# Optimization experiments

Measured on AMD Instinct MI355X. Metric: run time of the kernel, lower is better.

The kernel has to match this reference:

```python
import jax, jax.numpy as jnp
import numpy as np

EPS_LOG = 1e-08   # module eps (added inside log)
EPS_PD = 1e-06    # torch.nn.PairwiseDistance default eps (added to the difference)


def setup_inputs() -> dict:
    key = jax.random.key(0)
    x = jax.random.normal(key, (8192, 512), dtype=jnp.float32)
    return {"x": x}


def reference(x) -> jnp.ndarray:
    n = x.shape[0]
    # Cosine/dot similarity matrix [n, n]; mask the diagonal with -1 so a
    # point cannot be its own nearest neighbor.
    dots = x @ x.T
    idx = jnp.arange(n)
    dots = dots.at[idx, idx].set(-1.0)
    # Nearest neighbor (by dot product) per row; indices — no gradient path.
    I = jnp.argmax(dots, axis=1)
    # PairwiseDistance(p=2): ||x - x[I] + eps||_2 per row.
    diff = x - x[I] + EPS_PD
    rho = jnp.sqrt(jnp.sum(diff * diff, axis=1))
    loss = -jnp.mean(jnp.log(rho + EPS_LOG))
    return loss
```

## Files before the change

kernel.cpp:

```cpp
#include <hip/hip_runtime.h>


#define NPTS 8192
#define DIM  512
#define BM   128
#define BN   128
#define NTIL 64
#define NBLK (NTIL * (NTIL + 1) / 2)
#define KT_N 8

typedef float f32x16 __attribute__((ext_vector_type(16)));
typedef int   i32x4  __attribute__((ext_vector_type(4)));
typedef int   i32x8  __attribute__((ext_vector_type(8)));

__device__ __forceinline__ unsigned char f32_to_e4m3(float f) {
  unsigned u = __builtin_bit_cast(unsigned, f);
  unsigned s = (u >> 24) & 0x80u;
  unsigned a = u & 0x7FFFFFFFu;
  float af = __builtin_bit_cast(float, a);
  if (af < 0.015625f) {
    int m = (int)rintf(af * 512.0f);
    return (unsigned char)(s | (unsigned)m);
  }
  unsigned u2 = a + 0x0007FFFFu + ((a >> 20) & 1u);
  int e = (int)(u2 >> 23) - 127 + 7;
  unsigned m = (u2 >> 20) & 7u;
  if (e > 15) return (unsigned char)(s | 0x7Eu);
  return (unsigned char)(s | ((unsigned)e << 3) | m);
}

__device__ __forceinline__ unsigned int mono_f32(float f) {
  unsigned u = __builtin_bit_cast(unsigned, f);
  return u ^ (0x80000000u | (unsigned)((int)u >> 31));
}

__global__ void cvt_fp8_kernel(const float* __restrict__ x,
                               unsigned char* __restrict__ xq,
                               unsigned* __restrict__ nn32) {
  int i = blockIdx.x * blockDim.x + threadIdx.x;
  const float4* xp = reinterpret_cast<const float4*>(x) + 2 * (size_t)i;
  float4 v0 = xp[0], v1 = xp[1];
  unsigned long long w =
      (unsigned long long)f32_to_e4m3(v0.x) |
      ((unsigned long long)f32_to_e4m3(v0.y) << 8) |
      ((unsigned long long)f32_to_e4m3(v0.z) << 16) |
      ((unsigned long long)f32_to_e4m3(v0.w) << 24) |
      ((unsigned long long)f32_to_e4m3(v1.x) << 32) |
      ((unsigned long long)f32_to_e4m3(v1.y) << 40) |
      ((unsigned long long)f32_to_e4m3(v1.z) << 48) |
      ((unsigned long long)f32_to_e4m3(v1.w) << 56);
  reinterpret_cast<unsigned long long*>(xq)[i] = w;
  if (i < NPTS) nn32[i] = 0u;
}

__device__ __forceinline__ void gload_lds16(const unsigned char* g,
                                            unsigned char* l) {
  __builtin_amdgcn_global_load_lds(
      (__attribute__((address_space(1))) const void*)g,
      (__attribute__((address_space(3))) void*)l, 16, 0, 0);
}

__device__ __forceinline__ unsigned umax(unsigned a, unsigned b) {
  return a > b ? a : b;
}

__global__ __launch_bounds__(256, 3) void tri_gemm_kernel(
    const unsigned char* __restrict__ xq,
    unsigned* __restrict__ nn32) {
  __shared__ unsigned char lds[3][16384];

  const int orig = (int)blockIdx.x;
  int b = (orig & 7) * (NBLK >> 3) + (orig >> 3);
  int ti = (int)((sqrtf(8.0f * (float)b + 1.0f) - 1.0f) * 0.5f);
  while ((ti + 1) * (ti + 2) / 2 <= b) ++ti;
  while (ti * (ti + 1) / 2 > b) --ti;
  const int tj = b - ti * (ti + 1) / 2;

  const int tid  = (int)threadIdx.x;
  const int wid  = tid >> 6;
  const int lane = tid & 63;
  const int wr   = wid >> 1;
  const int wc   = wid & 1;
  const int l31  = lane & 31;
  const int h    = lane >> 5;
  const int arow0 = ti * BM;
  const int bcol0 = tj * BN;

#define STAGE(bufi, kt) do {                                                 \
    _Pragma("unroll")                                                        \
    for (int i_ = 0; i_ < 2; ++i_) {                                         \
      const int chunk_ = (i_ << 8) + tid;                        \
      const int row_   = chunk_ >> 2;                            \
      const int f_     = ((row_ >> 1) + (row_ >> 3)) & 3;                    \
      const int c_     = ((chunk_ & 3) - f_) & 3;                            \
      gload_lds16(xq + (size_t)(arow0 + row_) * DIM + (kt) * 64 + (c_ << 4), \
                  &lds[bufi][chunk_ << 4]);                                   \
      gload_lds16(xq + (size_t)(bcol0 + row_) * DIM + (kt) * 64 + (c_ << 4), \
                  &lds[bufi][8192 + (chunk_ << 4)]);                          \
    }                                                                        \
  } while (0)

  const int fr  = ((l31 >> 1) + (l31 >> 3)) & 3;
  const int s0  = (2 * h + fr) & 3;
  const int s1  = (2 * h + 1 + fr) & 3;
  const int abase = (wr * 64 + l31) * 64;
  const int bbase = 8192 + (wc * 64 + l31) * 64;
  const int aoff0 = abase + (s0 << 4), aoff1 = abase + (s1 << 4);
  const int boff0 = bbase + (s0 << 4), boff1 = bbase + (s1 << 4);

  f32x16 acc[2][2];
#pragma unroll
  for (int mi = 0; mi < 2; ++mi)
#pragma unroll
    for (int ni = 0; ni < 2; ++ni)
#pragma unroll
      for (int r = 0; r < 16; ++r) acc[mi][ni][r] = 0.f;

  STAGE(0, 0);
  STAGE(1, 1);

  for (int u = 0; u < KT_N; ++u) {
    const int cur = u - (u / 3) * 3;
    if (u == KT_N - 1) {
      asm volatile("s_waitcnt vmcnt(0)" ::: "memory");
    } else {
      asm volatile("s_waitcnt vmcnt(4)" ::: "memory");
    }
    asm volatile("s_barrier" ::: "memory");
    if (u + 2 < KT_N) {
      const int nb = (u + 2) - ((u + 2) / 3) * 3;
      STAGE(nb, u + 2);
    }

    i32x8 a8[2], b8[2];
#pragma unroll
    for (int mi = 0; mi < 2; ++mi) {
      i32x4 lo = *reinterpret_cast<const i32x4*>(&lds[cur][aoff0 + mi * 2048]);
      i32x4 hi = *reinterpret_cast<const i32x4*>(&lds[cur][aoff1 + mi * 2048]);
      a8[mi] = (i32x8){lo[0], lo[1], lo[2], lo[3], hi[0], hi[1], hi[2], hi[3]};
    }
#pragma unroll
    for (int ni = 0; ni < 2; ++ni) {
      i32x4 lo = *reinterpret_cast<const i32x4*>(&lds[cur][boff0 + ni * 2048]);
      i32x4 hi = *reinterpret_cast<const i32x4*>(&lds[cur][boff1 + ni * 2048]);
      b8[ni] = (i32x8){lo[0], lo[1], lo[2], lo[3], hi[0], hi[1], hi[2], hi[3]};
    }
    __builtin_amdgcn_s_setprio(1);
#pragma unroll
    for (int mi = 0; mi < 2; ++mi)
#pragma unroll
      for (int ni = 0; ni < 2; ++ni)
        acc[mi][ni] = __builtin_amdgcn_mfma_scale_f32_32x32x64_f8f6f4(
            a8[mi], b8[ni], acc[mi][ni], 0, 0,
            0, 0x7F7F7F7F, 0, 0x7F7F7F7F);
    __builtin_amdgcn_s_setprio(0);
  }
#undef STAGE

  const bool diagw = (ti == tj) && (wr == wc);

  unsigned M[2][2][16];
#pragma unroll
  for (int mi = 0; mi < 2; ++mi)
#pragma unroll
    for (int ni = 0; ni < 2; ++ni)
#pragma unroll
      for (int r = 0; r < 16; ++r)
        M[mi][ni][r] = mono_f32(acc[mi][ni][r]) & 0xFFFFE000u;

  unsigned K[32];
  const unsigned jb = 8191u - (unsigned)(bcol0 + wc * 64 + l31);
#pragma unroll
  for (int mi = 0; mi < 2; ++mi)
#pragma unroll
    for (int r = 0; r < 16; ++r) {
      const int rl = (r & 3) + 8 * (r >> 2) + 4 * h;
      unsigned best = 0u;
#pragma unroll
      for (int ni = 0; ni < 2; ++ni) {
        unsigned kk = M[mi][ni][r] | (jb - (unsigned)(ni * 32));
        if (diagw && mi == ni && rl == l31) kk = 0u;
        best = umax(best, kk);
      }
      K[mi * 16 + r] = best;
    }
#pragma unroll
  for (int k = 0; k < 5; ++k) {
    const int m = 1 << k;
    const unsigned kb = (unsigned)(lane >> k) & 1u;
#pragma unroll
    for (int i = 0; i < (16 >> k); ++i) {
      unsigned lo = K[2 * i], hi = K[2 * i + 1];
      unsigned keep = kb ? hi : lo;
      unsigned send = kb ? lo : hi;
      unsigned recv = (unsigned)__shfl_xor((int)send, m);
      K[i] = umax(keep, recv);
    }
  }
  {
    const int s = l31;
    const int gi = arow0 + wr * 64 + (s >> 4) * 32 +
                   ((s & 3) + 8 * ((s & 15) >> 2) + 4 * h);
    atomicMax(&nn32[gi], K[0]);
  }

  {
    unsigned C0 = 0u, C1 = 0u;
    const unsigned ib = 8191u - (unsigned)(arow0 + wr * 64);
#pragma unroll
    for (int mi = 0; mi < 2; ++mi)
#pragma unroll
      for (int r = 0; r < 16; ++r) {
        const int rl = (r & 3) + 8 * (r >> 2) + 4 * h;
        const unsigned idxk = ib - (unsigned)(mi * 32 + rl);
        unsigned k0 = M[mi][0][r] | idxk;
        if (diagw && mi == 0 && rl == l31) k0 = 0u;
        C0 = umax(C0, k0);
        unsigned k1 = M[mi][1][r] | idxk;
        if (diagw && mi == 1 && rl == l31) k1 = 0u;
        C1 = umax(C1, k1);
      }
    unsigned keep = h ? C1 : C0;
    unsigned send = h ? C0 : C1;
    unsigned recv = (unsigned)__shfl_xor((int)send, 32);
    unsigned R = umax(keep, recv);
    const int gj = bcol0 + wc * 64 + h * 32 + l31;
    atomicMax(&nn32[gj], R);
  }
}

__global__ void dist_log_kernel(const float* __restrict__ x,
                                const unsigned* __restrict__ nn32,
                                float* __restrict__ logs) {
  const int row  = blockIdx.x * 4 + ((int)threadIdx.x >> 6);
  const int lane = (int)threadIdx.x & 63;
  const int nn   = 8191 - (int)(nn32[row] & 8191u);
  const float4* xr = reinterpret_cast<const float4*>(x + (size_t)row * DIM);
  const float4* xn = reinterpret_cast<const float4*>(x + (size_t)nn  * DIM);
  float s = 0.f;
#pragma unroll
  for (int i = 0; i < 2; ++i) {
    float4 a = xr[lane + i * 64];
    float4 b = xn[lane + i * 64];
    float d0 = a.x - b.x + 1e-6f;
    float d1 = a.y - b.y + 1e-6f;
    float d2 = a.z - b.z + 1e-6f;
    float d3 = a.w - b.w + 1e-6f;
    s += d0 * d0 + d1 * d1 + d2 * d2 + d3 * d3;
  }
#pragma unroll
  for (int m = 32; m >= 1; m >>= 1) s += __shfl_xor(s, m);
  if (lane == 0) logs[row] = logf(sqrtf(s) + 1e-8f);
}

__global__ void final_reduce_kernel(const float* __restrict__ logs,
                                    float* __restrict__ out) {
  __shared__ float sm[1024];
  const int t = (int)threadIdx.x;
  float s = 0.f;
#pragma unroll
  for (int i = 0; i < 8; ++i) s += logs[t * 8 + i];
  sm[t] = s;
  __syncthreads();
  for (int k = 512; k > 0; k >>= 1) {
    if (t < k) sm[t] += sm[t + k];
    __syncthreads();
  }
  if (t == 0) out[0] = -(sm[0] / (float)NPTS);
}

extern "C" void kernel_launch(void* const* d_in, const int* in_sizes, int n_in,
                              void* d_out, int out_size, void* d_ws, size_t ws_size,
                              hipStream_t stream) {
  const float* x = (const float*)d_in[0];
  float* out = (float*)d_out;
  char* ws = (char*)d_ws;

  unsigned char* xq   = (unsigned char*)(ws);
  unsigned*      nn32 = (unsigned*)(ws + 4194304);
  float*         logs = (float*)(ws + 4227072);

  cvt_fp8_kernel<<<(NPTS * DIM / 8) / 256, 256, 0, stream>>>(x, xq, nn32);

  tri_gemm_kernel<<<NBLK, 256, 0, stream>>>(xq, nn32);

  dist_log_kernel<<<NPTS / 4, 256, 0, stream>>>(x, nn32, logs);

  final_reduce_kernel<<<1, 1024, 0, stream>>>(logs, out);
}
```

Before: 45.83 us.

## Switch K-loop to double-buffered 128-wide stages with fewer barriers

Replaces the triple-buffered 64-wide K pipeline (8 iterations, prefetch distance 2) with a double-buffered pipeline whose stages cover 128 bytes of K (4 iterations, prefetch distance 1). The goal is to halve the number of barriers and waitcnt points per tile and issue larger load batches. In exchange each iteration waits with vmcnt(0), so less load latency overlaps with compute, and LDS grows from 48KB to 64KB, which may cut occupancy below the three blocks per CU the launch bounds request.

```diff
diff --git a/kernel.cpp b/kernel.cpp
--- a/kernel.cpp
+++ b/kernel.cpp
@@ -7,7 +7,7 @@
 #define BN   128
 #define NTIL 64
 #define NBLK (NTIL * (NTIL + 1) / 2)
-#define KT_N 8
+#define MT_N 4
 
 typedef float f32x16 __attribute__((ext_vector_type(16)));
 typedef int   i32x4  __attribute__((ext_vector_type(4)));
@@ -67,7 +67,7 @@
 __global__ __launch_bounds__(256, 3) void tri_gemm_kernel(
     const unsigned char* __restrict__ xq,
     unsigned* __restrict__ nn32) {
-  __shared__ unsigned char lds[3][16384];
+  __shared__ unsigned char lds[2][32768];
 
   const int orig = (int)blockIdx.x;
   int b = (orig & 7) * (NBLK >> 3) + (orig >> 3);
@@ -86,17 +86,21 @@
   const int arow0 = ti * BM;
   const int bcol0 = tj * BN;
 
-#define STAGE(bufi, kt) do {                                                 \
+#define STAGE2(bufi, mt) do {                                                \
     _Pragma("unroll")                                                        \
-    for (int i_ = 0; i_ < 2; ++i_) {                                         \
-      const int chunk_ = (i_ << 8) + tid;                        \
-      const int row_   = chunk_ >> 2;                            \
-      const int f_     = ((row_ >> 1) + (row_ >> 3)) & 3;                    \
-      const int c_     = ((chunk_ & 3) - f_) & 3;                            \
-      gload_lds16(xq + (size_t)(arow0 + row_) * DIM + (kt) * 64 + (c_ << 4), \
-                  &lds[bufi][chunk_ << 4]);                                   \
-      gload_lds16(xq + (size_t)(bcol0 + row_) * DIM + (kt) * 64 + (c_ << 4), \
-                  &lds[bufi][8192 + (chunk_ << 4)]);                          \
+    for (int q_ = 0; q_ < 2; ++q_) {                                         \
+      _Pragma("unroll")                                                      \
+      for (int i_ = 0; i_ < 2; ++i_) {                                       \
+        const int chunk_ = (i_ << 8) + tid;                      \
+        const int row_   = chunk_ >> 2;                          \
+        const int f_     = ((row_ >> 1) + (row_ >> 3)) & 3;                  \
+        const int c_     = ((chunk_ & 3) - f_) & 3;                          \
+        const size_t go_ = (size_t)(mt) * 128 + q_ * 64 + (c_ << 4);         \
+        gload_lds16(xq + (size_t)(arow0 + row_) * DIM + go_,                 \
+                    &lds[bufi][q_ * 16384 + (chunk_ << 4)]);                  \
+        gload_lds16(xq + (size_t)(bcol0 + row_) * DIM + go_,                 \
+                    &lds[bufi][q_ * 16384 + 8192 + (chunk_ << 4)]);           \
+      }                                                                      \
     }                                                                        \
   } while (0)
 
@@ -116,46 +120,48 @@
 #pragma unroll
       for (int r = 0; r < 16; ++r) acc[mi][ni][r] = 0.f;
 
-  STAGE(0, 0);
-  STAGE(1, 1);
-
-  for (int u = 0; u < KT_N; ++u) {
-    const int cur = u - (u / 3) * 3;
-    if (u == KT_N - 1) {
-      asm volatile("s_waitcnt vmcnt(0)" ::: "memory");
-    } else {
-      asm volatile("s_waitcnt vmcnt(4)" ::: "memory");
+  STAGE2(0, 0);
+
+  for (int u = 0; u < MT_N; ++u) {
+    const int cur = u & 1;
+    asm volatile("s_waitcnt vmcnt(0)" ::: "memory");
+    asm volatile("s_barrier" ::: "memory");
+    if (u + 1 < MT_N) STAGE2(cur ^ 1, u + 1);
+
+#pragma unroll
+    for (int q = 0; q < 2; ++q) {
+      const int qb = q * 16384;
+      i32x8 a8[2], b8[2];
+#pragma unroll
+      for (int mi = 0; mi < 2; ++mi) {
+        i32x4 lo = *reinterpret_cast<const i32x4*>(
+            &lds[cur][qb + aoff0 + mi * 2048]);
+        i32x4 hi = *reinterpret_cast<const i32x4*>(
+            &lds[cur][qb + aoff1 + mi * 2048]);
+        a8[mi] = (i32x8){lo[0], lo[1], lo[2], lo[3],
+                         hi[0], hi[1], hi[2], hi[3]};
+      }
+#pragma unroll
+      for (int ni = 0; ni < 2; ++ni) {
+        i32x4 lo = *reinterpret_cast<const i32x4*>(
+            &lds[cur][qb + boff0 + ni * 2048]);
+        i32x4 hi = *reinterpret_cast<const i32x4*>(
+            &lds[cur][qb + boff1 + ni * 2048]);
+        b8[ni] = (i32x8){lo[0], lo[1], lo[2], lo[3],
+                         hi[0], hi[1], hi[2], hi[3]};
+      }
+      __builtin_amdgcn_s_setprio(1);
+#pragma unroll
+      for (int mi = 0; mi < 2; ++mi)
+#pragma unroll
+        for (int ni = 0; ni < 2; ++ni)
+          acc[mi][ni] = __builtin_amdgcn_mfma_scale_f32_32x32x64_f8f6f4(
+              a8[mi], b8[ni], acc[mi][ni], 0, 0,
+              0, 0x7F7F7F7F, 0, 0x7F7F7F7F);
+      __builtin_amdgcn_s_setprio(0);
     }
-    asm volatile("s_barrier" ::: "memory");
-    if (u + 2 < KT_N) {
-      const int nb = (u + 2) - ((u + 2) / 3) * 3;
-      STAGE(nb, u + 2);
-    }
-
-    i32x8 a8[2], b8[2];
-#pragma unroll
-    for (int mi = 0; mi < 2; ++mi) {
-      i32x4 lo = *reinterpret_cast<const i32x4*>(&lds[cur][aoff0 + mi * 2048]);
-      i32x4 hi = *reinterpret_cast<const i32x4*>(&lds[cur][aoff1 + mi * 2048]);
-      a8[mi] = (i32x8){lo[0], lo[1], lo[2], lo[3], hi[0], hi[1], hi[2], hi[3]};
-    }
-#pragma unroll
-    for (int ni = 0; ni < 2; ++ni) {
-      i32x4 lo = *reinterpret_cast<const i32x4*>(&lds[cur][boff0 + ni * 2048]);
-      i32x4 hi = *reinterpret_cast<const i32x4*>(&lds[cur][boff1 + ni * 2048]);
-      b8[ni] = (i32x8){lo[0], lo[1], lo[2], lo[3], hi[0], hi[1], hi[2], hi[3]};
-    }
-    __builtin_amdgcn_s_setprio(1);
-#pragma unroll
-    for (int mi = 0; mi < 2; ++mi)
-#pragma unroll
-      for (int ni = 0; ni < 2; ++ni)
-        acc[mi][ni] = __builtin_amdgcn_mfma_scale_f32_32x32x64_f8f6f4(
-            a8[mi], b8[ni], acc[mi][ni], 0, 0,
-            0, 0x7F7F7F7F, 0, 0x7F7F7F7F);
-    __builtin_amdgcn_s_setprio(0);
-  }
-#undef STAGE
+  }
+#undef STAGE2
 
   const bool diagw = (ti == tj) && (wr == wc);
 
```

Measured after the change: 50.33 us. +9.8%, slower.

## Switch triangular GEMM to single-wave 64x64 tiles with barrier-free double buffering

Applied to the files above, without the earlier changes.

Changes the triangular fp8 GEMM from 128x128 tiles run by four waves to 64x64 tiles run by one 64-lane wave, with a two-stage LDS buffer and no block barrier. Precomputed load pointers replace the per-stage address math, and the prefetch into the current buffer is issued after its LDS reads complete. The aim is to remove barrier sync and triangle-edge waste and to raise block count and occupancy. The cost is less operand reuse per block, so global and L2 traffic roughly doubles, and there are more atomicMax calls.

```diff
diff --git a/kernel.cpp b/kernel.cpp
--- a/kernel.cpp
+++ b/kernel.cpp
@@ -3,9 +3,8 @@
 
 #define NPTS 8192
 #define DIM  512
-#define BM   128
-#define BN   128
-#define NTIL 64
+#define BT   64
+#define NTIL 128
 #define NBLK (NTIL * (NTIL + 1) / 2)
 #define KT_N 8
 
@@ -64,10 +63,10 @@
   return a > b ? a : b;
 }
 
-__global__ __launch_bounds__(256, 3) void tri_gemm_kernel(
+__global__ __launch_bounds__(64, 3) void tri_gemm_kernel(
     const unsigned char* __restrict__ xq,
     unsigned* __restrict__ nn32) {
-  __shared__ unsigned char lds[3][16384];
+  __shared__ unsigned char lds[2][8192];
 
   const int orig = (int)blockIdx.x;
   int b = (orig & 7) * (NBLK >> 3) + (orig >> 3);
@@ -76,37 +75,39 @@
   while (ti * (ti + 1) / 2 > b) --ti;
   const int tj = b - ti * (ti + 1) / 2;
 
-  const int tid  = (int)threadIdx.x;
-  const int wid  = tid >> 6;
-  const int lane = tid & 63;
-  const int wr   = wid >> 1;
-  const int wc   = wid & 1;
+  const int lane = (int)threadIdx.x;
   const int l31  = lane & 31;
   const int h    = lane >> 5;
-  const int arow0 = ti * BM;
-  const int bcol0 = tj * BN;
+  const int arow0 = ti * BT;
+  const int bcol0 = tj * BT;
+
+  const unsigned char* pa[4];
+  const unsigned char* pb[4];
+  int ldst[4];
+#pragma unroll
+  for (int q = 0; q < 4; ++q) {
+    const int row = q * 16 + (lane >> 2);
+    const int f   = ((row >> 1) + (row >> 3)) & 3;
+    const int g   = ((lane & 3) - f) & 3;
+    pa[q] = xq + (size_t)(arow0 + row) * DIM + (g << 4);
+    pb[q] = xq + (size_t)(bcol0 + row) * DIM + (g << 4);
+    ldst[q] = ((q << 6) + lane) << 4;
+  }
 
 #define STAGE(bufi, kt) do {                                                 \
     _Pragma("unroll")                                                        \
-    for (int i_ = 0; i_ < 2; ++i_) {                                         \
-      const int chunk_ = (i_ << 8) + tid;                        \
-      const int row_   = chunk_ >> 2;                            \
-      const int f_     = ((row_ >> 1) + (row_ >> 3)) & 3;                    \
-      const int c_     = ((chunk_ & 3) - f_) & 3;                            \
-      gload_lds16(xq + (size_t)(arow0 + row_) * DIM + (kt) * 64 + (c_ << 4), \
-                  &lds[bufi][chunk_ << 4]);                                   \
-      gload_lds16(xq + (size_t)(bcol0 + row_) * DIM + (kt) * 64 + (c_ << 4), \
-                  &lds[bufi][8192 + (chunk_ << 4)]);                          \
+    for (int q_ = 0; q_ < 4; ++q_) {                                         \
+      gload_lds16(pa[q_] + (kt) * 64, &lds[bufi][ldst[q_]]);                 \
+      gload_lds16(pb[q_] + (kt) * 64, &lds[bufi][4096 + ldst[q_]]);          \
     }                                                                        \
   } while (0)
 
-  const int fr  = ((l31 >> 1) + (l31 >> 3)) & 3;
-  const int s0  = (2 * h + fr) & 3;
-  const int s1  = (2 * h + 1 + fr) & 3;
-  const int abase = (wr * 64 + l31) * 64;
-  const int bbase = 8192 + (wc * 64 + l31) * 64;
-  const int aoff0 = abase + (s0 << 4), aoff1 = abase + (s1 << 4);
-  const int boff0 = bbase + (s0 << 4), boff1 = bbase + (s1 << 4);
+  const int fr = ((l31 >> 1) + (l31 >> 3)) & 3;
+  const int s0 = (2 * h + fr) & 3;
+  const int s1 = (2 * h + 1 + fr) & 3;
+  const int aoff0 = l31 * 64 + (s0 << 4), aoff1 = l31 * 64 + (s1 << 4);
+  const int boff0 = 4096 + l31 * 64 + (s0 << 4);
+  const int boff1 = 4096 + l31 * 64 + (s1 << 4);
 
   f32x16 acc[2][2];
 #pragma unroll
@@ -119,32 +120,38 @@
   STAGE(0, 0);
   STAGE(1, 1);
 
-  for (int u = 0; u < KT_N; ++u) {
-    const int cur = u - (u / 3) * 3;
-    if (u == KT_N - 1) {
+#pragma unroll
+  for (int t = 0; t < KT_N; ++t) {
+    const int cur = t & 1;
+    if (t + 1 < KT_N) {
+      asm volatile("s_waitcnt vmcnt(8)" ::: "memory");
+    } else {
       asm volatile("s_waitcnt vmcnt(0)" ::: "memory");
-    } else {
-      asm volatile("s_waitcnt vmcnt(4)" ::: "memory");
-    }
-    asm volatile("s_barrier" ::: "memory");
-    if (u + 2 < KT_N) {
-      const int nb = (u + 2) - ((u + 2) / 3) * 3;
-      STAGE(nb, u + 2);
-    }
+    }
+
+    i32x4 al[2], ah[2], bl[2], bh[2];
+#pragma unroll
+    for (int mi = 0; mi < 2; ++mi) {
+      al[mi] = *reinterpret_cast<const i32x4*>(&lds[cur][aoff0 + mi * 2048]);
+      ah[mi] = *reinterpret_cast<const i32x4*>(&lds[cur][aoff1 + mi * 2048]);
+    }
+#pragma unroll
+    for (int ni = 0; ni < 2; ++ni) {
+      bl[ni] = *reinterpret_cast<const i32x4*>(&lds[cur][boff0 + ni * 2048]);
+      bh[ni] = *reinterpret_cast<const i32x4*>(&lds[cur][boff1 + ni * 2048]);
+    }
+    asm volatile("s_waitcnt lgkmcnt(0)" ::: "memory");
+    if (t + 2 < KT_N) STAGE(cur, t + 2);
 
     i32x8 a8[2], b8[2];
 #pragma unroll
-    for (int mi = 0; mi < 2; ++mi) {
-      i32x4 lo = *reinterpret_cast<const i32x4*>(&lds[cur][aoff0 + mi * 2048]);
-      i32x4 hi = *reinterpret_cast<const i32x4*>(&lds[cur][aoff1 + mi * 2048]);
-      a8[mi] = (i32x8){lo[0], lo[1], lo[2], lo[3], hi[0], hi[1], hi[2], hi[3]};
-    }
-#pragma unroll
-    for (int ni = 0; ni < 2; ++ni) {
-      i32x4 lo = *reinterpret_cast<const i32x4*>(&lds[cur][boff0 + ni * 2048]);
-      i32x4 hi = *reinterpret_cast<const i32x4*>(&lds[cur][boff1 + ni * 2048]);
-      b8[ni] = (i32x8){lo[0], lo[1], lo[2], lo[3], hi[0], hi[1], hi[2], hi[3]};
-    }
+    for (int mi = 0; mi < 2; ++mi)
+      a8[mi] = (i32x8){al[mi][0], al[mi][1], al[mi][2], al[mi][3],
+                       ah[mi][0], ah[mi][1], ah[mi][2], ah[mi][3]};
+#pragma unroll
+    for (int ni = 0; ni < 2; ++ni)
+      b8[ni] = (i32x8){bl[ni][0], bl[ni][1], bl[ni][2], bl[ni][3],
+                       bh[ni][0], bh[ni][1], bh[ni][2], bh[ni][3]};
     __builtin_amdgcn_s_setprio(1);
 #pragma unroll
     for (int mi = 0; mi < 2; ++mi)
@@ -157,7 +164,7 @@
   }
 #undef STAGE
 
-  const bool diagw = (ti == tj) && (wr == wc);
+  const bool diagw = (ti == tj);
 
   unsigned M[2][2][16];
 #pragma unroll
@@ -169,7 +176,7 @@
         M[mi][ni][r] = mono_f32(acc[mi][ni][r]) & 0xFFFFE000u;
 
   unsigned K[32];
-  const unsigned jb = 8191u - (unsigned)(bcol0 + wc * 64 + l31);
+  const unsigned jb = 8191u - (unsigned)(bcol0 + l31);
 #pragma unroll
   for (int mi = 0; mi < 2; ++mi)
 #pragma unroll
@@ -199,14 +206,14 @@
   }
   {
     const int s = l31;
-    const int gi = arow0 + wr * 64 + (s >> 4) * 32 +
+    const int gi = arow0 + (s >> 4) * 32 +
                    ((s & 3) + 8 * ((s & 15) >> 2) + 4 * h);
     atomicMax(&nn32[gi], K[0]);
   }
 
   {
     unsigned C0 = 0u, C1 = 0u;
-    const unsigned ib = 8191u - (unsigned)(arow0 + wr * 64);
+    const unsigned ib = 8191u - (unsigned)arow0;
 #pragma unroll
     for (int mi = 0; mi < 2; ++mi)
 #pragma unroll
@@ -224,7 +231,7 @@
     unsigned send = h ? C0 : C1;
     unsigned recv = (unsigned)__shfl_xor((int)send, 32);
     unsigned R = umax(keep, recv);
-    const int gj = bcol0 + wc * 64 + h * 32 + l31;
+    const int gj = bcol0 + h * 32 + l31;
     atomicMax(&nn32[gj], R);
   }
 }
@@ -282,7 +289,7 @@
 
   cvt_fp8_kernel<<<(NPTS * DIM / 8) / 256, 256, 0, stream>>>(x, xq, nn32);
 
-  tri_gemm_kernel<<<NBLK, 256, 0, stream>>>(xq, nn32);
+  tri_gemm_kernel<<<NBLK, 64, 0, stream>>>(xq, nn32);
 
   dist_log_kernel<<<NPTS / 4, 256, 0, stream>>>(x, nn32, logs);
 
```

After: 53.33 us. +16.4%, slower.
